# Performance work log

Hardware: AMD Instinct MI355X
Metric: run time of the kernel (lower is better)

Reference implementation:

```python
import jax, jax.numpy as jnp
import numpy as np

D_MODEL = 1024
HEADS = 16
D_K = D_MODEL // HEADS
B, S = 2, 2048
NEG = -1000000000.0

def setup_inputs() -> dict:
    key = jax.random.key(0)
    ks = jax.random.split(key, 11)
    sc = 1.0 / np.sqrt(D_MODEL)
    inp = {
        'q': jax.random.normal(ks[0], (B, S, D_MODEL), jnp.float32),
        'k': jax.random.normal(ks[1], (B, S, D_MODEL), jnp.float32),
        'v': jax.random.normal(ks[2], (B, S, D_MODEL), jnp.float32),
        'mask': jnp.tril(jnp.ones((S, S), jnp.int32))[None, None],  # causal [1,1,S,S]
        'wq_w': jax.random.normal(ks[3], (D_MODEL, D_MODEL), jnp.float32) * sc,
        'wq_b': jax.random.normal(ks[4], (D_MODEL,), jnp.float32) * 0.02,
        'wk_w': jax.random.normal(ks[5], (D_MODEL, D_MODEL), jnp.float32) * sc,
        'wk_b': jax.random.normal(ks[6], (D_MODEL,), jnp.float32) * 0.02,
        'wv_w': jax.random.normal(ks[7], (D_MODEL, D_MODEL), jnp.float32) * sc,
        'wv_b': jax.random.normal(ks[8], (D_MODEL,), jnp.float32) * 0.02,
        'wo_w': jax.random.normal(ks[9], (D_MODEL, D_MODEL), jnp.float32) * sc,
        'wo_b': jax.random.normal(ks[10], (D_MODEL,), jnp.float32) * 0.02,
    }
    return inp

def reference(q, k, v, mask, wq_w, wq_b, wk_w, wk_b, wv_w, wv_b, wo_w, wo_b):
    b, s, _ = q.shape
    # projections (torch Linear: x @ W^T + b)
    Q = (q @ wq_w.T + wq_b).reshape(b, s, HEADS, D_K).transpose(0, 2, 1, 3)  # [B,H,S,Dk]
    K = (k @ wk_w.T + wk_b).reshape(b, s, HEADS, D_K).transpose(0, 2, 1, 3)
    V = (v @ wv_w.T + wv_b).reshape(b, s, HEADS, D_K).transpose(0, 2, 1, 3)
    scores = jnp.einsum('bhqd,bhkd->bhqk', Q, K) / jnp.sqrt(jnp.float32(D_K))
    scores = jnp.where(mask == 0, NEG, scores)
    p = jax.nn.softmax(scores, axis=-1)  # dropout=0.0 -> identity
    x = jnp.einsum('bhqk,bhkd->bhqd', p, V)
    x = x.transpose(0, 2, 1, 3).reshape(b, s, D_MODEL)
    return x @ wo_w.T + wo_b
```

## Files before the change

### kernel.cpp

```cpp
#include <hip/hip_runtime.h>

typedef unsigned short u16;
typedef __attribute__((ext_vector_type(8))) short bf16x8;
typedef __attribute__((ext_vector_type(4))) float f32x4;

#define SEQ 2048
#define DMODEL 1024

__device__ __forceinline__ u16 f2bf(float f) {
    union { float f; unsigned u; } x; x.f = f;
    unsigned r = x.u + 0x7fffu + ((x.u >> 16) & 1u);
    return (u16)(r >> 16);
}

__device__ __forceinline__ u16 f2bf_trunc(float f) {
    union { float f; unsigned u; } x; x.f = f;
    return (u16)(x.u >> 16);
}

__device__ __forceinline__ float bf2f(u16 v) {
    union { unsigned u; float f; } x; x.u = ((unsigned)v) << 16;
    return x.f;
}

__device__ __forceinline__ f32x4 mfma16(bf16x8 a, bf16x8 b, f32x4 c) {
    return __builtin_amdgcn_mfma_f32_16x16x32_bf16(a, b, c, 0, 0, 0);
}

__device__ __forceinline__ void gld16(const u16* g, u16* l) {
    __builtin_amdgcn_global_load_lds(
        (__attribute__((address_space(1))) const void*)g,
        (__attribute__((address_space(3))) void*)l, 16, 0, 0);
}

struct CvtArgs {
    const float* src[7];
    u16* dst[7];
    int n4[7];
};

__global__ __launch_bounds__(256) void cvt_kernel(CvtArgs a) {
    const int id = blockIdx.y;
    const int i = blockIdx.x * 256 + threadIdx.x;
    if (i >= a.n4[id]) return;
    float4 f = ((const float4*)a.src[id])[i];
    ushort4 u;
    u.x = f2bf(f.x); u.y = f2bf(f.y); u.z = f2bf(f.z); u.w = f2bf(f.w);
    ((ushort4*)a.dst[id])[i] = u;
}

__global__ __launch_bounds__(256) void gemm_qkv(
    const u16* __restrict__ Xq, const u16* __restrict__ Xk, const u16* __restrict__ Xv,
    const u16* __restrict__ Wq, const u16* __restrict__ Wk, const u16* __restrict__ Wv,
    const float* __restrict__ bq, const float* __restrict__ bk, const float* __restrict__ bv,
    u16* __restrict__ Qb, u16* __restrict__ Kb, u16* __restrict__ Vb)
{
    const int bid = blockIdx.x;
    const int xcd = bid & 7;
    const int li  = bid >> 3;
    const int nb_ = li / 12;
    const int mloc = li % 12;
    const int gm  = xcd * 12 + mloc;
    const int z   = gm >> 5;
    const int bm  = (gm & 31) * 128;
    const int bn  = nb_ * 128;

    const u16* X = (z == 0) ? Xq : (z == 1) ? Xk : Xv;
    const u16* W = (z == 0) ? Wq : (z == 1) ? Wk : Wv;
    const float* bias = (z == 0) ? bq : (z == 1) ? bk : bv;

    __shared__ u16 As[128 * 32];
    __shared__ u16 Bs[128 * 32];

    const int tid = threadIdx.x;
    const int lane = tid & 63, w = tid >> 6;
    const int wm = (w >> 1) * 64, wn = (w & 1) * 64;
    const int r = lane & 15, qd = lane >> 4;

    const int cb0 = w * 64;
    const int cb1 = 256 + w * 64;
    const int c0 = cb0 + lane, c1 = cb1 + lane;
    const int r0 = c0 >> 2, o0 = (c0 & 3) * 8;
    const int r1 = c1 >> 2, o1 = (c1 & 3) * 8;

    f32x4 acc[4][4];
    #pragma unroll
    for (int i = 0; i < 4; ++i)
        #pragma unroll
        for (int j = 0; j < 4; ++j)
            acc[i][j] = (f32x4){0.f, 0.f, 0.f, 0.f};

    for (int kk = 0; kk < 1024; kk += 32) {
        __syncthreads();
        gld16(X + (size_t)(bm + r0) * 1024 + kk + o0, As + cb0 * 8);
        gld16(X + (size_t)(bm + r1) * 1024 + kk + o1, As + cb1 * 8);
        gld16(W + (size_t)(bn + r0) * 1024 + kk + o0, Bs + cb0 * 8);
        gld16(W + (size_t)(bn + r1) * 1024 + kk + o1, Bs + cb1 * 8);
        __syncthreads();

        bf16x8 aF[4], bF[4];
        #pragma unroll
        for (int i = 0; i < 4; ++i)
            aF[i] = *(const bf16x8*)(As + (wm + i * 16 + r) * 32 + qd * 8);
        #pragma unroll
        for (int j = 0; j < 4; ++j)
            bF[j] = *(const bf16x8*)(Bs + (wn + j * 16 + r) * 32 + qd * 8);
        #pragma unroll
        for (int i = 0; i < 4; ++i)
            #pragma unroll
            for (int j = 0; j < 4; ++j)
                acc[i][j] = mfma16(aF[i], bF[j], acc[i][j]);
    }

    const float scale = (z == 0) ? 0.125f : 1.0f;
    #pragma unroll
    for (int j = 0; j < 4; ++j) {
        const int n = bn + wn + j * 16 + r;
        const float bvl = bias[n];
        const int h = n >> 6, d = n & 63;
        #pragma unroll
        for (int i = 0; i < 4; ++i) {
            const int m0 = bm + wm + i * 16 + qd * 4;
            const int b_ = m0 >> 11, s0 = m0 & 2047;
            if (z == 0) {
                #pragma unroll
                for (int reg = 0; reg < 4; ++reg)
                    Qb[(size_t)(m0 + reg) * 1024 + n] = f2bf((acc[i][j][reg] + bvl) * scale);
            } else if (z == 1) {
                #pragma unroll
                for (int reg = 0; reg < 4; ++reg)
                    Kb[((size_t)(b_ * 16 + h) * SEQ + s0 + reg) * 64 + d] =
                        f2bf(acc[i][j][reg] + bvl);
            } else {
                ushort4 u;
                u.x = f2bf(acc[i][j][0] + bvl);
                u.y = f2bf(acc[i][j][1] + bvl);
                u.z = f2bf(acc[i][j][2] + bvl);
                u.w = f2bf(acc[i][j][3] + bvl);
                *(ushort4*)(Vb + ((size_t)(b_ * 16 + h) * 64 + d) * SEQ + s0) = u;
            }
        }
    }
}

__global__ __launch_bounds__(128, 3) void attn_kernel(
    const u16* __restrict__ Qb, const u16* __restrict__ Kb,
    const u16* __restrict__ Vb, u16* __restrict__ Op, float* __restrict__ Lp)
{
    __shared__ u16 Kst[2][4096];
    __shared__ u16 Vst[2][4096];
    __shared__ u16 Pst[2][16 * 72];

    const int bid = blockIdx.x;
    const int xcd = bid & 7;
    const int i2 = bid >> 3;
    const int bh = xcd + 8 * (i2 & 3);
    const int rest = i2 >> 2;
    const int g = 31 - (rest >> 1);
    const int half = rest & 1;
    const int b_ = bh >> 4, h = bh & 15;

    const int h0 = (g + 1) >> 1;
    const int j0 = half ? h0 : 0;
    const int j1 = half ? (g + 1) : h0;

    const int tid = threadIdx.x;
    const int lane = tid & 63, w = tid >> 6;
    const int r = lane & 15, qd = lane >> 4;

    const u16* Kh = Kb + (size_t)bh * SEQ * 64;
    const u16* Vh = Vb + (size_t)bh * 64 * SEQ;
    u16* Pw = Pst[w];

    bf16x8 aQ[2][2];
    #pragma unroll
    for (int i = 0; i < 2; ++i) {
        const size_t qoff =
            (size_t)(b_ * SEQ + g * 64 + w * 32 + i * 16 + r) * DMODEL + h * 64;
        aQ[i][0] = *(const bf16x8*)(Qb + qoff + qd * 8);
        aQ[i][1] = *(const bf16x8*)(Qb + qoff + 32 + qd * 8);
    }

    bf16x8 ones;
    #pragma unroll
    for (int e = 0; e < 8; ++e) ones[e] = (short)0x3F80;

    f32x4 o[2][4];
    f32x4 l[2];
    #pragma unroll
    for (int i = 0; i < 2; ++i) {
        l[i] = (f32x4){0.f, 0.f, 0.f, 0.f};
        #pragma unroll
        for (int db = 0; db < 4; ++db) o[i][db] = (f32x4){0.f, 0.f, 0.f, 0.f};
    }

    auto stage = [&](int j, int buf) {
        if (w == 0) {
            const u16* Kt = Kh + (size_t)j * 64 * 64;
            #pragma unroll
            for (int s = 0; s < 8; ++s)
                gld16(Kt + ((s >> 1) * 16 + r) * 64 + (s & 1) * 32 + qd * 8,
                      &Kst[buf][s * 512]);
        } else {
            const u16* Vt = Vh + j * 64;
            #pragma unroll
            for (int s = 0; s < 8; ++s)
                gld16(Vt + (size_t)((s >> 1) * 16 + r) * SEQ + (s & 1) * 32 + qd * 8,
                      &Vst[buf][s * 512]);
        }
    };

    if (j0 < j1) stage(j0, j0 & 1);

    for (int j = j0; j < j1; ++j) {
        const int cur = j & 1;
        __syncthreads();
        if (j + 1 < j1) stage(j + 1, 1 - cur);

        bf16x8 kf[4][2], vf[4][2];
        #pragma unroll
        for (int nb = 0; nb < 4; ++nb) {
            kf[nb][0] = *(const bf16x8*)(&Kst[cur][(nb * 2 + 0) * 512 + lane * 8]);
            kf[nb][1] = *(const bf16x8*)(&Kst[cur][(nb * 2 + 1) * 512 + lane * 8]);
        }
        #pragma unroll
        for (int db = 0; db < 4; ++db) {
            vf[db][0] = *(const bf16x8*)(&Vst[cur][(db * 2 + 0) * 512 + lane * 8]);
            vf[db][1] = *(const bf16x8*)(&Vst[cur][(db * 2 + 1) * 512 + lane * 8]);
        }

        #pragma unroll
        for (int i = 0; i < 2; ++i) {
            f32x4 sc[4];
            #pragma unroll
            for (int nb = 0; nb < 4; ++nb) {
                f32x4 s = (f32x4){0.f, 0.f, 0.f, 0.f};
                s = mfma16(kf[nb][0], aQ[i][0], s);
                s = mfma16(kf[nb][1], aQ[i][1], s);
                sc[nb] = s;
            }

            if (j == g) {
                const int rowr = w * 32 + i * 16 + r;
                #pragma unroll
                for (int nb = 0; nb < 4; ++nb)
                    #pragma unroll
                    for (int reg = 0; reg < 4; ++reg)
                        if (nb * 16 + qd * 4 + reg > rowr) sc[nb][reg] = -1e30f;
            }

            #pragma unroll
            for (int nb = 0; nb < 4; ++nb)
                #pragma unroll
                for (int reg = 0; reg < 4; ++reg)
                    sc[nb][reg] = exp2f(fmaf(sc[nb][reg], 1.4426950408889634f,
                                             -23.083120654223414f));

            #pragma unroll
            for (int nb = 0; nb < 4; ++nb) {
                ushort4 pk;
                pk.x = f2bf_trunc(sc[nb][0]);
                pk.y = f2bf_trunc(sc[nb][1]);
                pk.z = f2bf_trunc(sc[nb][2]);
                pk.w = f2bf_trunc(sc[nb][3]);
                *(ushort4*)(Pw + r * 72 + nb * 16 + qd * 4) = pk;
            }

            const bf16x8 aP0 = *(const bf16x8*)(Pw + r * 72 + qd * 8);
            const bf16x8 aP1 = *(const bf16x8*)(Pw + r * 72 + 32 + qd * 8);

            l[i] = mfma16(aP0, ones, l[i]);
            l[i] = mfma16(aP1, ones, l[i]);

            #pragma unroll
            for (int db = 0; db < 4; ++db) {
                o[i][db] = mfma16(aP0, vf[db][0], o[i][db]);
                o[i][db] = mfma16(aP1, vf[db][1], o[i][db]);
            }
        }
    }

    u16* Oh = Op + ((size_t)(half * 1024 + bh * 32 + g) * 4096);
    float* Lh = Lp + (size_t)(half * 1024 + bh * 32 + g) * 64;
    #pragma unroll
    for (int i = 0; i < 2; ++i) {
        #pragma unroll
        for (int db = 0; db < 4; ++db)
            #pragma unroll
            for (int reg = 0; reg < 4; ++reg)
                Oh[(w * 32 + i * 16 + qd * 4 + reg) * 64 + db * 16 + r] =
                    f2bf(o[i][db][reg]);
        if (r == 0) {
            #pragma unroll
            for (int reg = 0; reg < 4; ++reg)
                Lh[w * 32 + i * 16 + qd * 4 + reg] = l[i][reg];
        }
    }
}

__global__ __launch_bounds__(256) void attn_norm(
    const u16* __restrict__ Op, const float* __restrict__ Lp,
    u16* __restrict__ AO)
{
    const int idx = blockIdx.x * 256 + threadIdx.x;
    const int col8 = idx & 127;
    const int row = idx >> 7;
    const int h = col8 >> 3;
    const int b_ = row >> 11, s = row & 2047;
    const int g = s >> 6, r64 = s & 63;
    const int bh = b_ * 16 + h;

    const size_t pa = ((size_t)(bh * 32 + g) * 4096) + r64 * 64 + (col8 & 7) * 8;
    const size_t pb = pa + (size_t)1024 * 4096;
    const float la = Lp[(bh * 32 + g) * 64 + r64];
    const float lb = Lp[(1024 + bh * 32 + g) * 64 + r64];
    const float inv = 1.0f / (la + lb);

    const bf16x8 a = *(const bf16x8*)(Op + pa);
    const bf16x8 b = *(const bf16x8*)(Op + pb);
    bf16x8 o;
    #pragma unroll
    for (int e = 0; e < 8; ++e)
        o[e] = (short)f2bf((bf2f((u16)a[e]) + bf2f((u16)b[e])) * inv);
    *(bf16x8*)(AO + (size_t)row * 1024 + col8 * 8) = o;
}

__global__ __launch_bounds__(256) void gemm_out(
    const u16* __restrict__ AO, const u16* __restrict__ W,
    const float* __restrict__ bias, float* __restrict__ out)
{
    const int bid = blockIdx.x;
    const int xcd = bid & 7;
    const int li = bid >> 3;
    const int bn = (li >> 2) * 128;
    const int bm = (xcd * 4 + (li & 3)) * 128;

    __shared__ u16 As[128 * 32];
    __shared__ u16 Bs[128 * 32];

    const int tid = threadIdx.x;
    const int lane = tid & 63, w = tid >> 6;
    const int wm = (w >> 1) * 64, wn = (w & 1) * 64;
    const int r = lane & 15, qd = lane >> 4;

    const int cb0 = w * 64;
    const int cb1 = 256 + w * 64;
    const int c0 = cb0 + lane, c1 = cb1 + lane;
    const int r0 = c0 >> 2, o0 = (c0 & 3) * 8;
    const int r1 = c1 >> 2, o1 = (c1 & 3) * 8;

    f32x4 acc[4][4];
    #pragma unroll
    for (int i = 0; i < 4; ++i)
        #pragma unroll
        for (int j = 0; j < 4; ++j)
            acc[i][j] = (f32x4){0.f, 0.f, 0.f, 0.f};

    for (int kk = 0; kk < 1024; kk += 32) {
        __syncthreads();
        gld16(AO + (size_t)(bm + r0) * 1024 + kk + o0, As + cb0 * 8);
        gld16(AO + (size_t)(bm + r1) * 1024 + kk + o1, As + cb1 * 8);
        gld16(W + (size_t)(bn + r0) * 1024 + kk + o0, Bs + cb0 * 8);
        gld16(W + (size_t)(bn + r1) * 1024 + kk + o1, Bs + cb1 * 8);
        __syncthreads();

        bf16x8 aF[4], bF[4];
        #pragma unroll
        for (int i = 0; i < 4; ++i)
            aF[i] = *(const bf16x8*)(As + (wm + i * 16 + r) * 32 + qd * 8);
        #pragma unroll
        for (int j = 0; j < 4; ++j)
            bF[j] = *(const bf16x8*)(Bs + (wn + j * 16 + r) * 32 + qd * 8);
        #pragma unroll
        for (int i = 0; i < 4; ++i)
            #pragma unroll
            for (int j = 0; j < 4; ++j)
                acc[i][j] = mfma16(aF[i], bF[j], acc[i][j]);
    }

    #pragma unroll
    for (int j = 0; j < 4; ++j) {
        const int n = bn + wn + j * 16 + r;
        const float bvl = bias[n];
        #pragma unroll
        for (int i = 0; i < 4; ++i) {
            const int m0 = bm + wm + i * 16 + qd * 4;
            #pragma unroll
            for (int reg = 0; reg < 4; ++reg)
                out[(size_t)(m0 + reg) * 1024 + n] = acc[i][j][reg] + bvl;
        }
    }
}

extern "C" void kernel_launch(void* const* d_in, const int* in_sizes, int n_in,
                              void* d_out, int out_size, void* d_ws, size_t ws_size,
                              hipStream_t stream) {
    const float* q  = (const float*)d_in[0];
    const float* k  = (const float*)d_in[1];
    const float* v  = (const float*)d_in[2];
    const float* wq = (const float*)d_in[4];
    const float* bq = (const float*)d_in[5];
    const float* wk = (const float*)d_in[6];
    const float* bk = (const float*)d_in[7];
    const float* wv = (const float*)d_in[8];
    const float* bv = (const float*)d_in[9];
    const float* wo = (const float*)d_in[10];
    const float* bo = (const float*)d_in[11];
    float* out = (float*)d_out;

    u16* ws = (u16*)d_ws;
    u16* Xq = ws;
    u16* Xk = Xq + (size_t)4194304;
    u16* Xv = Xk + (size_t)4194304;
    u16* Wq = Xv + (size_t)4194304;
    u16* Wk = Wq + (size_t)1048576;
    u16* Wv = Wk + (size_t)1048576;
    u16* Wo = Wv + (size_t)1048576;
    u16* Qb = Wo + (size_t)1048576;
    u16* Kb = Qb + (size_t)4194304;
    u16* Vb = Kb + (size_t)4194304;
    u16* AO = Vb + (size_t)4194304;

    u16* Op = ws;
    float* Lp = (float*)(ws + (size_t)8388608);

    CvtArgs ca;
    ca.src[0] = q;  ca.dst[0] = Xq; ca.n4[0] = 1048576;
    ca.src[1] = k;  ca.dst[1] = Xk; ca.n4[1] = 1048576;
    ca.src[2] = v;  ca.dst[2] = Xv; ca.n4[2] = 1048576;
    ca.src[3] = wq; ca.dst[3] = Wq; ca.n4[3] = 262144;
    ca.src[4] = wk; ca.dst[4] = Wk; ca.n4[4] = 262144;
    ca.src[5] = wv; ca.dst[5] = Wv; ca.n4[5] = 262144;
    ca.src[6] = wo; ca.dst[6] = Wo; ca.n4[6] = 262144;

    cvt_kernel<<<dim3(4096, 7), 256, 0, stream>>>(ca);
    gemm_qkv<<<dim3(768), 256, 0, stream>>>(Xq, Xk, Xv, Wq, Wk, Wv,
                                            bq, bk, bv, Qb, Kb, Vb);
    attn_kernel<<<dim3(2048), 128, 0, stream>>>(Qb, Kb, Vb, Op, Lp);
    attn_norm<<<dim3(2048), 256, 0, stream>>>(Op, Lp, AO);
    gemm_out<<<dim3(256), 256, 0, stream>>>(AO, Wo, bo, out);
}
```

Measured before the change: 255.6 us.

## Rewrite projection GEMMs with 256x256 tiles, double-buffered swizzled LDS pipeline

Both the QKV and output projection GEMMs move from 128x128 tiles with a K-step of 32 to 256x256 tiles with a K-step of 64 and 512 threads. They now use double-buffered LDS staging with an XOR swizzle, explicit waitcnt/barrier pipelining and setprio around the MFMA bursts. The aim is more operand reuse, hiding global-load latency and avoiding LDS bank conflicts. The trade-off is fewer blocks (192 and 64), which leaves many CUs idle and risks underutilisation, especially in the output GEMM.

New measurement: 258.3 us. About the same (+1.1%).

```diff
diff --git a/kernel.cpp b/kernel.cpp
--- a/kernel.cpp
+++ b/kernel.cpp
@@ -49,78 +49,114 @@
     ((ushort4*)a.dst[id])[i] = u;
 }
 
-__global__ __launch_bounds__(256) void gemm_qkv(
+
+__global__ __launch_bounds__(512, 2) void gemm_qkv(
     const u16* __restrict__ Xq, const u16* __restrict__ Xk, const u16* __restrict__ Xv,
     const u16* __restrict__ Wq, const u16* __restrict__ Wk, const u16* __restrict__ Wv,
     const float* __restrict__ bq, const float* __restrict__ bk, const float* __restrict__ bv,
     u16* __restrict__ Qb, u16* __restrict__ Kb, u16* __restrict__ Vb)
 {
+    __shared__ u16 Abuf[2][256 * 64];
+    __shared__ u16 Bbuf[2][256 * 64];
+
     const int bid = blockIdx.x;
-    const int xcd = bid & 7;
-    const int li  = bid >> 3;
-    const int nb_ = li / 12;
-    const int mloc = li % 12;
-    const int gm  = xcd * 12 + mloc;
-    const int z   = gm >> 5;
-    const int bm  = (gm & 31) * 128;
-    const int bn  = nb_ * 128;
+    const int G = (bid & 7) * 24 + (bid >> 3);
+    const int z = G >> 6;
+    const int rem = G & 63;
+    const int bm = (rem >> 2) * 256;
+    const int bn = (rem & 3) * 256;
 
     const u16* X = (z == 0) ? Xq : (z == 1) ? Xk : Xv;
     const u16* W = (z == 0) ? Wq : (z == 1) ? Wk : Wv;
     const float* bias = (z == 0) ? bq : (z == 1) ? bk : bv;
 
-    __shared__ u16 As[128 * 32];
-    __shared__ u16 Bs[128 * 32];
-
     const int tid = threadIdx.x;
     const int lane = tid & 63, w = tid >> 6;
-    const int wm = (w >> 1) * 64, wn = (w & 1) * 64;
+    const int wr = w >> 2, wc = w & 3;
     const int r = lane & 15, qd = lane >> 4;
 
-    const int cb0 = w * 64;
-    const int cb1 = 256 + w * 64;
-    const int c0 = cb0 + lane, c1 = cb1 + lane;
-    const int r0 = c0 >> 2, o0 = (c0 & 3) * 8;
-    const int r1 = c1 >> 2, o1 = (c1 & 3) * 8;
-
-    f32x4 acc[4][4];
-    #pragma unroll
-    for (int i = 0; i < 4; ++i)
+    const int srow = lane >> 3;
+    const int scol = ((lane & 7) ^ srow) * 8;
+    const u16* Xs = X + (size_t)(bm + w * 32 + srow) * 1024 + scol;
+    const u16* Ws = W + (size_t)(bn + w * 32 + srow) * 1024 + scol;
+
+    const int rxor = (r & 7) << 4;
+    const int rowA = (wr * 128 + r) * 128;
+    const int rowB = (wc * 64 + r) * 128;
+    const int ko0 = (qd * 16) ^ rxor;
+    const int ko1 = (64 + qd * 16) ^ rxor;
+
+    f32x4 acc[8][4];
+    #pragma unroll
+    for (int i = 0; i < 8; ++i)
         #pragma unroll
         for (int j = 0; j < 4; ++j)
             acc[i][j] = (f32x4){0.f, 0.f, 0.f, 0.f};
 
-    for (int kk = 0; kk < 1024; kk += 32) {
-        __syncthreads();
-        gld16(X + (size_t)(bm + r0) * 1024 + kk + o0, As + cb0 * 8);
-        gld16(X + (size_t)(bm + r1) * 1024 + kk + o1, As + cb1 * 8);
-        gld16(W + (size_t)(bn + r0) * 1024 + kk + o0, Bs + cb0 * 8);
-        gld16(W + (size_t)(bn + r1) * 1024 + kk + o1, Bs + cb1 * 8);
-        __syncthreads();
-
-        bf16x8 aF[4], bF[4];
-        #pragma unroll
-        for (int i = 0; i < 4; ++i)
-            aF[i] = *(const bf16x8*)(As + (wm + i * 16 + r) * 32 + qd * 8);
-        #pragma unroll
-        for (int j = 0; j < 4; ++j)
-            bF[j] = *(const bf16x8*)(Bs + (wn + j * 16 + r) * 32 + qd * 8);
-        #pragma unroll
-        for (int i = 0; i < 4; ++i)
-            #pragma unroll
-            for (int j = 0; j < 4; ++j)
-                acc[i][j] = mfma16(aF[i], bF[j], acc[i][j]);
+    auto stage = [&](int t) {
+        const int d = t & 1;
+        const u16* xa = Xs + t * 64;
+        const u16* wb = Ws + t * 64;
+        u16* Al = &Abuf[d][w * 2048];
+        u16* Bl = &Bbuf[d][w * 2048];
+        #pragma unroll
+        for (int q = 0; q < 4; ++q) {
+            gld16(xa + (size_t)q * 8192, Al + q * 512);
+            gld16(wb + (size_t)q * 8192, Bl + q * 512);
+        }
+    };
+
+    stage(0);
+    stage(1);
+    asm volatile("s_waitcnt vmcnt(8)" ::: "memory");
+    __builtin_amdgcn_sched_barrier(0);
+    __builtin_amdgcn_s_barrier();
+
+    for (int t = 0; t < 16; ++t) {
+        const u16* Ab = Abuf[t & 1];
+        const u16* Bb = Bbuf[t & 1];
+        #pragma unroll
+        for (int kc = 0; kc < 2; ++kc) {
+            const int ko = kc ? ko1 : ko0;
+            bf16x8 aF[8], bF[4];
+            #pragma unroll
+            for (int m = 0; m < 8; ++m)
+                aF[m] = *(const bf16x8*)((const char*)Ab + rowA + m * 2048 + ko);
+            #pragma unroll
+            for (int n = 0; n < 4; ++n)
+                bF[n] = *(const bf16x8*)((const char*)Bb + rowB + n * 2048 + ko);
+            __builtin_amdgcn_s_setprio(1);
+            #pragma unroll
+            for (int m = 0; m < 8; ++m)
+                #pragma unroll
+                for (int n = 0; n < 4; ++n)
+                    acc[m][n] = mfma16(aF[m], bF[n], acc[m][n]);
+            __builtin_amdgcn_s_setprio(0);
+        }
+        if (t == 15) break;
+        asm volatile("s_waitcnt lgkmcnt(0)" ::: "memory");
+        __builtin_amdgcn_sched_barrier(0);
+        __builtin_amdgcn_s_barrier();
+        if (t < 14) {
+            stage(t + 2);
+            asm volatile("s_waitcnt vmcnt(8)" ::: "memory");
+        } else {
+            asm volatile("s_waitcnt vmcnt(0)" ::: "memory");
+        }
+        __builtin_amdgcn_sched_barrier(0);
+        __builtin_amdgcn_s_barrier();
+        __builtin_amdgcn_sched_barrier(0);
     }
 
     const float scale = (z == 0) ? 0.125f : 1.0f;
     #pragma unroll
     for (int j = 0; j < 4; ++j) {
-        const int n = bn + wn + j * 16 + r;
+        const int n = bn + wc * 64 + j * 16 + r;
         const float bvl = bias[n];
         const int h = n >> 6, d = n & 63;
         #pragma unroll
-        for (int i = 0; i < 4; ++i) {
-            const int m0 = bm + wm + i * 16 + qd * 4;
+        for (int i = 0; i < 8; ++i) {
+            const int m0 = bm + wr * 128 + i * 16 + qd * 4;
             const int b_ = m0 >> 11, s0 = m0 & 2047;
             if (z == 0) {
                 #pragma unroll
@@ -325,66 +361,103 @@
     *(bf16x8*)(AO + (size_t)row * 1024 + col8 * 8) = o;
 }
 
-__global__ __launch_bounds__(256) void gemm_out(
+__global__ __launch_bounds__(512, 2) void gemm_out(
     const u16* __restrict__ AO, const u16* __restrict__ W,
     const float* __restrict__ bias, float* __restrict__ out)
 {
+    __shared__ u16 Abuf[2][256 * 64];
+    __shared__ u16 Bbuf[2][256 * 64];
+
     const int bid = blockIdx.x;
-    const int xcd = bid & 7;
-    const int li = bid >> 3;
-    const int bn = (li >> 2) * 128;
-    const int bm = (xcd * 4 + (li & 3)) * 128;
-
-    __shared__ u16 As[128 * 32];
-    __shared__ u16 Bs[128 * 32];
+    const int G = (bid & 7) * 8 + (bid >> 3);
+    const int bm = (G >> 2) * 256;
+    const int bn = (G & 3) * 256;
 
     const int tid = threadIdx.x;
     const int lane = tid & 63, w = tid >> 6;
-    const int wm = (w >> 1) * 64, wn = (w & 1) * 64;
+    const int wr = w >> 2, wc = w & 3;
     const int r = lane & 15, qd = lane >> 4;
 
-    const int cb0 = w * 64;
-    const int cb1 = 256 + w * 64;
-    const int c0 = cb0 + lane, c1 = cb1 + lane;
-    const int r0 = c0 >> 2, o0 = (c0 & 3) * 8;
-    const int r1 = c1 >> 2, o1 = (c1 & 3) * 8;
-
-    f32x4 acc[4][4];
-    #pragma unroll
-    for (int i = 0; i < 4; ++i)
+    const int srow = lane >> 3;
+    const int scol = ((lane & 7) ^ srow) * 8;
+    const u16* Xs = AO + (size_t)(bm + w * 32 + srow) * 1024 + scol;
+    const u16* Ws = W + (size_t)(bn + w * 32 + srow) * 1024 + scol;
+
+    const int rxor = (r & 7) << 4;
+    const int rowA = (wr * 128 + r) * 128;
+    const int rowB = (wc * 64 + r) * 128;
+    const int ko0 = (qd * 16) ^ rxor;
+    const int ko1 = (64 + qd * 16) ^ rxor;
+
+    f32x4 acc[8][4];
+    #pragma unroll
+    for (int i = 0; i < 8; ++i)
         #pragma unroll
         for (int j = 0; j < 4; ++j)
             acc[i][j] = (f32x4){0.f, 0.f, 0.f, 0.f};
 
-    for (int kk = 0; kk < 1024; kk += 32) {
-        __syncthreads();
-        gld16(AO + (size_t)(bm + r0) * 1024 + kk + o0, As + cb0 * 8);
-        gld16(AO + (size_t)(bm + r1) * 1024 + kk + o1, As + cb1 * 8);
-        gld16(W + (size_t)(bn + r0) * 1024 + kk + o0, Bs + cb0 * 8);
-        gld16(W + (size_t)(bn + r1) * 1024 + kk + o1, Bs + cb1 * 8);
-        __syncthreads();
-
-        bf16x8 aF[4], bF[4];
-        #pragma unroll
-        for (int i = 0; i < 4; ++i)
-            aF[i] = *(const bf16x8*)(As + (wm + i * 16 + r) * 32 + qd * 8);
-        #pragma unroll
-        for (int j = 0; j < 4; ++j)
-            bF[j] = *(const bf16x8*)(Bs + (wn + j * 16 + r) * 32 + qd * 8);
-        #pragma unroll
-        for (int i = 0; i < 4; ++i)
-            #pragma unroll
-            for (int j = 0; j < 4; ++j)
-                acc[i][j] = mfma16(aF[i], bF[j], acc[i][j]);
+    auto stage = [&](int t) {
+        const int d = t & 1;
+        const u16* xa = Xs + t * 64;
+        const u16* wb = Ws + t * 64;
+        u16* Al = &Abuf[d][w * 2048];
+        u16* Bl = &Bbuf[d][w * 2048];
+        #pragma unroll
+        for (int q = 0; q < 4; ++q) {
+            gld16(xa + (size_t)q * 8192, Al + q * 512);
+            gld16(wb + (size_t)q * 8192, Bl + q * 512);
+        }
+    };
+
+    stage(0);
+    stage(1);
+    asm volatile("s_waitcnt vmcnt(8)" ::: "memory");
+    __builtin_amdgcn_sched_barrier(0);
+    __builtin_amdgcn_s_barrier();
+
+    for (int t = 0; t < 16; ++t) {
+        const u16* Ab = Abuf[t & 1];
+        const u16* Bb = Bbuf[t & 1];
+        #pragma unroll
+        for (int kc = 0; kc < 2; ++kc) {
+            const int ko = kc ? ko1 : ko0;
+            bf16x8 aF[8], bF[4];
+            #pragma unroll
+            for (int m = 0; m < 8; ++m)
+                aF[m] = *(const bf16x8*)((const char*)Ab + rowA + m * 2048 + ko);
+            #pragma unroll
+            for (int n = 0; n < 4; ++n)
+                bF[n] = *(const bf16x8*)((const char*)Bb + rowB + n * 2048 + ko);
+            __builtin_amdgcn_s_setprio(1);
+            #pragma unroll
+            for (int m = 0; m < 8; ++m)
+                #pragma unroll
+                for (int n = 0; n < 4; ++n)
+                    acc[m][n] = mfma16(aF[m], bF[n], acc[m][n]);
+            __builtin_amdgcn_s_setprio(0);
+        }
+        if (t == 15) break;
+        asm volatile("s_waitcnt lgkmcnt(0)" ::: "memory");
+        __builtin_amdgcn_sched_barrier(0);
+        __builtin_amdgcn_s_barrier();
+        if (t < 14) {
+            stage(t + 2);
+            asm volatile("s_waitcnt vmcnt(8)" ::: "memory");
+        } else {
+            asm volatile("s_waitcnt vmcnt(0)" ::: "memory");
+        }
+        __builtin_amdgcn_sched_barrier(0);
+        __builtin_amdgcn_s_barrier();
+        __builtin_amdgcn_sched_barrier(0);
     }
 
     #pragma unroll
     for (int j = 0; j < 4; ++j) {
-        const int n = bn + wn + j * 16 + r;
+        const int n = bn + wc * 64 + j * 16 + r;
         const float bvl = bias[n];
         #pragma unroll
-        for (int i = 0; i < 4; ++i) {
-            const int m0 = bm + wm + i * 16 + qd * 4;
+        for (int i = 0; i < 8; ++i) {
+            const int m0 = bm + wr * 128 + i * 16 + qd * 4;
             #pragma unroll
             for (int reg = 0; reg < 4; ++reg)
                 out[(size_t)(m0 + reg) * 1024 + n] = acc[i][j][reg] + bvl;
@@ -434,9 +507,9 @@
     ca.src[6] = wo; ca.dst[6] = Wo; ca.n4[6] = 262144;
 
     cvt_kernel<<<dim3(4096, 7), 256, 0, stream>>>(ca);
-    gemm_qkv<<<dim3(768), 256, 0, stream>>>(Xq, Xk, Xv, Wq, Wk, Wv,
+    gemm_qkv<<<dim3(192), 512, 0, stream>>>(Xq, Xk, Xv, Wq, Wk, Wv,
                                             bq, bk, bv, Qb, Kb, Vb);
     attn_kernel<<<dim3(2048), 128, 0, stream>>>(Qb, Kb, Vb, Op, Lp);
     attn_norm<<<dim3(2048), 256, 0, stream>>>(Op, Lp, AO);
-    gemm_out<<<dim3(256), 256, 0, stream>>>(AO, Wo, bo, out);
-}
+    gemm_out<<<dim3(256 / 4), 512, 0, stream>>>(AO, Wo, bo, out);
+}
```
